# Kernel optimization log

Measured on AMD Instinct MI355X. Metric: run time of the kernel, lower is better.

## Reference

```python
import jax, jax.numpy as jnp
import numpy as np

H = 8        # attention heads
EPS = 1e-5   # LayerNorm eps (torch default)


def _ln(x, g, b):
    m = x.mean(-1, keepdims=True)
    v = ((x - m) ** 2).mean(-1, keepdims=True)
    return (x - m) / jnp.sqrt(v + EPS) * g + b


def _mha(q, k, v):
    # q,k,v: [B, A, S, D] -> attend over S within each (B, A); D = H * dh
    Bq, A, S, Dm = q.shape
    dh = Dm // H
    q = q.reshape(Bq, A, S, H, dh)
    k = k.reshape(Bq, A, S, H, dh)
    v = v.reshape(Bq, A, S, H, dh)
    sc = jnp.einsum('bashe,bathe->bahst', q, k) / jnp.sqrt(jnp.asarray(dh, q.dtype))
    a = jax.nn.softmax(sc, axis=-1)
    o = jnp.einsum('bahst,bathe->bashe', a, v)
    return o.reshape(Bq, A, S, Dm)


def setup_inputs() -> dict:
    Ps, B, C, L, D, DF, PRED = 6, 16, 8, 64, 512, 2048, 96
    key = jax.random.key(0)
    ks = jax.random.split(key, 16)
    g = lambda k, s: jax.random.normal(k, s, jnp.float32) * 0.02
    D2 = (D, D)
    return dict(
        expert_x=jax.random.normal(ks[0], (Ps, B, C, L, D), jnp.float32),
        gates=jax.random.uniform(ks[1], (B, Ps), dtype=jnp.float32),
        cWq=g(ks[2], D2), cbq=jnp.zeros(D), cWk=g(ks[3], D2), cbk=jnp.zeros(D),
        cWv=g(ks[4], D2), cbv=jnp.zeros(D), cWo=g(ks[5], D2), cbo=jnp.zeros(D),
        iWq=g(ks[6], D2), ibq=jnp.zeros(D), iWk=g(ks[7], D2), ibk=jnp.zeros(D),
        iWv=g(ks[8], D2), ibv=jnp.zeros(D), iWo=g(ks[9], D2), ibo=jnp.zeros(D),
        mW1=g(ks[10], (D, DF)), mb1=jnp.zeros(DF),
        mW2=g(ks[11], (DF, D)), mb2=jnp.zeros(D),
        g1=jnp.ones(D), b1=jnp.zeros(D),
        g3=jnp.ones(D), b3=jnp.zeros(D),
        g4=jnp.ones(D), b4=jnp.zeros(D),
        hW=g(ks[12], (D, PRED)), hb=jnp.zeros(PRED),
    )


def reference(expert_x, gates,
              cWq, cbq, cWk, cbk, cWv, cbv, cWo, cbo,
              iWq, ibq, iWk, ibk, iWv, ibv, iWo, ibo,
              mW1, mb1, mW2, mb2,
              g1, b1, g3, b3, g4, b4,
              hW, hb):
    def layer(x):  # x: [B, C, L, D]
        # cross-dimension attention block (attend along L per channel)
        q = x @ cWq + cbq
        k = x @ cWk + cbk
        v = x @ cWv + cbv
        o = _mha(q, k, v) @ cWo + cbo
        x = _ln(x + o, g1, b1)
        # inter-periodicity attention block (rearrange B C L D -> B L C D, attend along C)
        q = (x @ iWq + ibq).swapaxes(1, 2)
        k = (x @ iWk + ibk).swapaxes(1, 2)
        v = (x @ iWv + ibv).swapaxes(1, 2)
        o = _mha(q, k, v).swapaxes(1, 2) @ iWo + ibo
        x = _ln(x + o, g3, b3)
        # inter-periodicity MLP (relu) + residual + norm4
        h = jnp.maximum(x @ mW1 + mb1, 0.0) @ mW2 + mb2
        return _ln(x + h, g4, b4)

    enc = jax.vmap(layer)(expert_x)                      # [Ps, B, C, L, D]
    last = enc[:, :, :, -1, :]                           # [Ps, B, C, D]: xs[i][:, :, -1:, :]
    combined = jnp.einsum('pbcd,bp->bcd', last, gates)   # gated combine over experts
    out = combined @ hW + hb                             # [B, C, pred_len]
    return out.transpose(0, 2, 1)                        # [B, pred_len, C]
```

## Files before the change

kernel.cpp:

```cpp
#include <hip/hip_runtime.h>
#include <hip/hip_bf16.h>

#define NT   49152
#define D_   512
#define DF_  2048
#define PS   6
#define BB   16
#define CC   8
#define LL   64
#define PREDN 96
#define NG   768

typedef unsigned short ushort_t;
using bf16x8 = __attribute__((ext_vector_type(8))) short;
using f32x4  = __attribute__((ext_vector_type(4))) float;

__device__ __forceinline__ float bf2f(unsigned short u) {
  return __uint_as_float((unsigned)u << 16);
}
__device__ __forceinline__ unsigned short f2bf(float f) {
  unsigned u = __float_as_uint(f);
  return (unsigned short)((u + 0x7fffu + ((u >> 16) & 1u)) >> 16);
}
__device__ __forceinline__ void unp2(int x, float& a, float& b) {
  a = __uint_as_float((unsigned)x << 16);
  b = __uint_as_float((unsigned)x & 0xffff0000u);
}
__device__ __forceinline__ void gload16(const void* g, void* l) {
  __builtin_amdgcn_global_load_lds(
      (const __attribute__((address_space(1))) unsigned*)g,
      (__attribute__((address_space(3))) unsigned*)l, 16, 0, 0);
}

template <bool RELU>
__global__ __launch_bounds__(512, 2) void gemm_mfma(
    const ushort_t* __restrict__ A,
    const ushort_t* __restrict__ Bt,
    const float* __restrict__ bias,
    ushort_t* __restrict__ C,
    int M, int N, int K) {
  __shared__ __align__(16) char smem[73728];
  short* lds = (short*)smem;
  const int tid = threadIdx.x;
  const int lane = tid & 63;
  const int w = tid >> 6;
  const int wm = w >> 1;
  const int wn = w & 1;
  const int l15 = lane & 15, l4 = lane >> 4;

  const int nbn = N >> 7;
  const int nwg = gridDim.x;
  const int qq = nwg >> 3, rr = nwg & 7;
  const int xcd = blockIdx.x & 7, within = blockIdx.x >> 3;
  const int wg = (xcd < rr ? xcd * (qq + 1) : rr * (qq + 1) + (xcd - rr) * qq) + within;
  const int bn = (wg % nbn) << 7;
  const int bm = (wg / nbn) << 8;

  const int NKT = K >> 5;

  const int ciA0 = w * 64 + lane;
  const int ciA1 = 512 + w * 64 + lane;
  const int ciB  = w * 64 + lane;
  const int rA0 = ciA0 >> 2, rA1 = ciA1 >> 2, rB = ciB >> 2;
  const int jA0 = (ciA0 & 3) ^ ((rA0 >> 1) & 3);
  const int jA1 = (ciA1 & 3) ^ ((rA1 >> 1) & 3);
  const int jB  = (ciB  & 3) ^ ((rB  >> 1) & 3);
  const ushort_t* gA0 = A + (size_t)(bm + rA0) * K + (jA0 << 3);
  const ushort_t* gA1 = A + (size_t)(bm + rA1) * K + (jA1 << 3);
  const ushort_t* gB  = Bt + (size_t)(bn + rB) * K + (jB << 3);

  auto stage = [&](int st, int sb) {
    const int k0 = st << 5;
    gload16(gA0 + k0, smem + sb * 24576 + w * 1024);
    gload16(gA1 + k0, smem + sb * 24576 + 8192 + w * 1024);
    gload16(gB  + k0, smem + sb * 24576 + 16384 + w * 1024);
  };

  int aconst[4], bconst[4];
#pragma unroll
  for (int m = 0; m < 4; ++m) {
    int row = wm * 64 + m * 16 + l15;
    aconst[m] = row * 32 + ((l4 ^ ((row >> 1) & 3)) << 3);
  }
#pragma unroll
  for (int n = 0; n < 4; ++n) {
    int row = wn * 64 + n * 16 + l15;
    bconst[n] = 8192 + row * 32 + ((l4 ^ ((row >> 1) & 3)) << 3);
  }

  f32x4 acc[4][4] = {};

  stage(0, 0);
  stage(1, 1);

  int rb = 0, sb = 2;
  for (int kt = 0; kt < NKT; ++kt) {
    asm volatile("s_waitcnt vmcnt(3)" ::: "memory");
    __builtin_amdgcn_s_barrier();
    const short* buf = lds + rb * 12288;
    bf16x8 av[4], bv[4];
#pragma unroll
    for (int m = 0; m < 4; ++m) av[m] = *(const bf16x8*)(buf + aconst[m]);
#pragma unroll
    for (int n = 0; n < 4; ++n) bv[n] = *(const bf16x8*)(buf + bconst[n]);
    const int st = (kt + 2 < NKT) ? kt + 2 : NKT - 1;
    stage(st, sb);
    __builtin_amdgcn_s_barrier();
    __builtin_amdgcn_s_setprio(1);
#pragma unroll
    for (int m = 0; m < 4; ++m)
#pragma unroll
      for (int n = 0; n < 4; ++n)
        acc[m][n] = __builtin_amdgcn_mfma_f32_16x16x32_bf16(av[m], bv[n], acc[m][n], 0, 0, 0);
    __builtin_amdgcn_s_setprio(0);
    rb = (rb == 2) ? 0 : rb + 1;
    sb = (sb == 2) ? 0 : sb + 1;
  }

  asm volatile("s_waitcnt vmcnt(0)" ::: "memory");
  __syncthreads();

  float bc[4];
#pragma unroll
  for (int n = 0; n < 4; ++n) bc[n] = bias[bn + wn * 64 + n * 16 + l15];
  short* Cs = lds;
#pragma unroll
  for (int m = 0; m < 4; ++m)
#pragma unroll
    for (int n = 0; n < 4; ++n)
#pragma unroll
      for (int r2 = 0; r2 < 4; ++r2) {
        float v = acc[m][n][r2] + bc[n];
        if (RELU) v = fmaxf(v, 0.f);
        Cs[(wm * 64 + m * 16 + l4 * 4 + r2) * 136 + wn * 64 + n * 16 + l15] =
            (short)f2bf(v);
      }
  __syncthreads();
#pragma unroll
  for (int it = 0; it < 8; ++it) {
    int chunk = it * 512 + tid;
    int r = chunk >> 4;
    int c = (chunk & 15) << 3;
    int4 v = *(const int4*)(Cs + r * 136 + c);
    *(int4*)(C + (size_t)(bm + r) * N + bn + c) = v;
  }
}

__global__ __launch_bounds__(256) void transpose8(
    const float* s0, const float* s1, const float* s2, const float* s3,
    const float* s4, const float* s5, const float* s6, const float* s7,
    ushort_t* d0, ushort_t* d1, ushort_t* d2, ushort_t* d3,
    ushort_t* d4, ushort_t* d5, ushort_t* d6, ushort_t* d7) {
  const float* srcs[8] = {s0, s1, s2, s3, s4, s5, s6, s7};
  ushort_t* dsts[8] = {d0, d1, d2, d3, d4, d5, d6, d7};
  const float* __restrict__ W = srcs[blockIdx.z];
  ushort_t* __restrict__ Wt = dsts[blockIdx.z];
  __shared__ float tile[32][33];
  const int k0 = blockIdx.x * 32, n0 = blockIdx.y * 32;
  const int tx = threadIdx.x & 31, ty = threadIdx.x >> 5;
#pragma unroll
  for (int i = 0; i < 4; ++i)
    tile[ty + i * 8][tx] = W[(size_t)(k0 + ty + i * 8) * 512 + n0 + tx];
  __syncthreads();
#pragma unroll
  for (int i = 0; i < 4; ++i)
    Wt[(size_t)(n0 + ty + i * 8) * 512 + k0 + tx] = f2bf(tile[tx][ty + i * 8]);
}

__global__ __launch_bounds__(256) void transpose_bf16(
    const float* __restrict__ W, ushort_t* __restrict__ Wt, int K, int N) {
  __shared__ float tile[32][33];
  const int k0 = blockIdx.x * 32, n0 = blockIdx.y * 32;
  const int tx = threadIdx.x & 31, ty = threadIdx.x >> 5;
#pragma unroll
  for (int i = 0; i < 4; ++i)
    tile[ty + i * 8][tx] = W[(size_t)(k0 + ty + i * 8) * N + n0 + tx];
  __syncthreads();
#pragma unroll
  for (int i = 0; i < 4; ++i)
    Wt[(size_t)(n0 + ty + i * 8) * K + k0 + tx] = f2bf(tile[tx][ty + i * 8]);
}

__global__ __launch_bounds__(256) void build_wqk(
    const float* __restrict__ cWk, ushort_t* __restrict__ Wqk) {
  int idx = blockIdx.x * 256 + threadIdx.x;
  int n = idx >> 6;
  int c = (idx & 63) * 8;
  int h = n >> 9, k = n & 511;
  union { unsigned short u[8]; int4 v; } pk;
  if ((c >> 6) == h) {
    float4 a = *(const float4*)(cWk + (size_t)k * 512 + c);
    float4 b = *(const float4*)(cWk + (size_t)k * 512 + c + 4);
    pk.u[0] = f2bf(a.x); pk.u[1] = f2bf(a.y); pk.u[2] = f2bf(a.z); pk.u[3] = f2bf(a.w);
    pk.u[4] = f2bf(b.x); pk.u[5] = f2bf(b.y); pk.u[6] = f2bf(b.z); pk.u[7] = f2bf(b.w);
  } else {
    pk.v = make_int4(0, 0, 0, 0);
  }
  *(int4*)(Wqk + (size_t)n * 512 + c) = pk.v;
}

__global__ __launch_bounds__(256) void bias_pack(
    const float* __restrict__ ibq, const float* __restrict__ ibk,
    const float* __restrict__ ibv, float* __restrict__ biqkv,
    float* __restrict__ qz) {
  int i = blockIdx.x * 256 + threadIdx.x;
  if (i < 512) biqkv[i] = ibq[i];
  else if (i < 1024) biqkv[i] = ibk[i - 512];
  else if (i < 1536) biqkv[i] = ibv[i - 1024];
  else if (i < 1536 + 4096) qz[i - 1536] = 0.f;
}

__global__ __launch_bounds__(64) void gather_conv(
    const float* __restrict__ ex, ushort_t* __restrict__ G) {
  const int g = blockIdx.x, lane = threadIdx.x;
  const float* src = ex + ((size_t)g * 64 + 63) * 512 + lane * 8;
  float4 a = *(const float4*)src, b = *(const float4*)(src + 4);
  union { unsigned short u[8]; int4 v; } pk;
  pk.u[0] = f2bf(a.x); pk.u[1] = f2bf(a.y); pk.u[2] = f2bf(a.z); pk.u[3] = f2bf(a.w);
  pk.u[4] = f2bf(b.x); pk.u[5] = f2bf(b.y); pk.u[6] = f2bf(b.z); pk.u[7] = f2bf(b.w);
  *(int4*)(G + (size_t)g * 512 + lane * 8) = pk.v;
}

__global__ __launch_bounds__(256) void attn_fused(
    const float* __restrict__ ex, const ushort_t* __restrict__ QW,
    ushort_t* __restrict__ Y) {
  __shared__ short xs[64][520];
  __shared__ short qws[8][520];
  __shared__ float ss[8][72];
  __shared__ float ps[8][72];
  const int g = blockIdx.x;
  const int tid = threadIdx.x;

  {
    const float* src = ex + (size_t)g * 64 * 512;
#pragma unroll
    for (int it = 0; it < 16; ++it) {
      int i = it * 256 + tid;
      int r = i >> 6, c = (i & 63) * 8;
      float4 a = *(const float4*)(src + r * 512 + c);
      float4 b = *(const float4*)(src + r * 512 + c + 4);
      union { unsigned short u[8]; int4 v; } pk;
      pk.u[0] = f2bf(a.x); pk.u[1] = f2bf(a.y); pk.u[2] = f2bf(a.z); pk.u[3] = f2bf(a.w);
      pk.u[4] = f2bf(b.x); pk.u[5] = f2bf(b.y); pk.u[6] = f2bf(b.z); pk.u[7] = f2bf(b.w);
      *(int4*)(&xs[r][c]) = pk.v;
    }
    const ushort_t* qsrc = QW + (size_t)g * 4096;
#pragma unroll
    for (int it = 0; it < 2; ++it) {
      int i = it * 256 + tid;
      int h = i >> 6, k0 = (i & 63) * 8;
      *(int4*)(&qws[h][k0]) = *(const int4*)(qsrc + i * 8);
    }
  }
  __syncthreads();

#pragma unroll
  for (int ph = 0; ph < 2; ++ph) {
    int h = tid & 7, t = (tid >> 3) + ph * 32;
    float s0 = 0.f, s1 = 0.f, s2 = 0.f, s3 = 0.f;
    float s4 = 0.f, s5 = 0.f, s6 = 0.f, s7 = 0.f;
#pragma unroll
    for (int k8 = 0; k8 < 64; ++k8) {
      bf16x8 xv = *(const bf16x8*)(&xs[t][k8 * 8]);
      bf16x8 qv = *(const bf16x8*)(&qws[h][k8 * 8]);
      s0 += bf2f((unsigned short)xv[0]) * bf2f((unsigned short)qv[0]);
      s1 += bf2f((unsigned short)xv[1]) * bf2f((unsigned short)qv[1]);
      s2 += bf2f((unsigned short)xv[2]) * bf2f((unsigned short)qv[2]);
      s3 += bf2f((unsigned short)xv[3]) * bf2f((unsigned short)qv[3]);
      s4 += bf2f((unsigned short)xv[4]) * bf2f((unsigned short)qv[4]);
      s5 += bf2f((unsigned short)xv[5]) * bf2f((unsigned short)qv[5]);
      s6 += bf2f((unsigned short)xv[6]) * bf2f((unsigned short)qv[6]);
      s7 += bf2f((unsigned short)xv[7]) * bf2f((unsigned short)qv[7]);
    }
    ss[h][t] = (((s0 + s1) + (s2 + s3)) + ((s4 + s5) + (s6 + s7))) * 0.125f;
  }
  __syncthreads();

  {
    int h = tid >> 5, t0 = tid & 31;
    float v0 = ss[h][t0], v1 = ss[h][t0 + 32];
    float mx = fmaxf(v0, v1);
#pragma unroll
    for (int o = 16; o > 0; o >>= 1) mx = fmaxf(mx, __shfl_xor(mx, o));
    float e0 = __expf(v0 - mx), e1 = __expf(v1 - mx);
    float sum = e0 + e1;
#pragma unroll
    for (int o = 16; o > 0; o >>= 1) sum += __shfl_xor(sum, o);
    float inv = 1.f / sum;
    ps[h][t0] = e0 * inv;
    ps[h][t0 + 32] = e1 * inv;
  }
  __syncthreads();

  {
    int h = tid >> 5, k0 = (tid & 31) * 16;
    float acc[16] = {};
#pragma unroll
    for (int t = 0; t < 64; ++t) {
      float p = ps[h][t];
      bf16x8 x0 = *(const bf16x8*)(&xs[t][k0]);
      bf16x8 x1 = *(const bf16x8*)(&xs[t][k0 + 8]);
#pragma unroll
      for (int j = 0; j < 8; ++j) {
        acc[j]     += p * bf2f((unsigned short)x0[j]);
        acc[8 + j] += p * bf2f((unsigned short)x1[j]);
      }
    }
    union { unsigned short u[16]; int4 v[2]; } pk;
#pragma unroll
    for (int j = 0; j < 16; ++j) pk.u[j] = f2bf(acc[j]);
    ushort_t* dst = Y + ((size_t)g * 8 + h) * 512 + k0;
    *(int4*)dst = pk.v[0];
    *(int4*)(dst + 8) = pk.v[1];
  }
}

__global__ __launch_bounds__(64) void gather_diag(
    const ushort_t* __restrict__ T, ushort_t* __restrict__ O) {
  const int g = blockIdx.x;
  const int n0 = threadIdx.x * 8;
  const int h = n0 >> 6;
  *(int4*)(O + (size_t)g * 512 + n0) =
      *(const int4*)(T + ((size_t)g * 8 + h) * 512 + n0);
}

__global__ __launch_bounds__(64) void attn_ctx(
    const ushort_t* __restrict__ QKV, ushort_t* __restrict__ O) {
  __shared__ float qs[8][72], ks[8][72], vsm[8][72], ps2[8][9];
  const int h = blockIdx.x & 7;
  const int pb = blockIdx.x >> 3;
  const int row0 = pb * 8;
  const int tid = threadIdx.x;
  {
    int c = tid >> 3, dc = (tid & 7) * 8;
    size_t r = (size_t)(row0 + c) * 1536 + h * 64 + dc;
    int4 qv = *(const int4*)(QKV + r);
    int4 kv = *(const int4*)(QKV + r + 512);
    int4 vv = *(const int4*)(QKV + r + 1024);
    unp2(qv.x, qs[c][dc + 0], qs[c][dc + 1]); unp2(qv.y, qs[c][dc + 2], qs[c][dc + 3]);
    unp2(qv.z, qs[c][dc + 4], qs[c][dc + 5]); unp2(qv.w, qs[c][dc + 6], qs[c][dc + 7]);
    unp2(kv.x, ks[c][dc + 0], ks[c][dc + 1]); unp2(kv.y, ks[c][dc + 2], ks[c][dc + 3]);
    unp2(kv.z, ks[c][dc + 4], ks[c][dc + 5]); unp2(kv.w, ks[c][dc + 6], ks[c][dc + 7]);
    unp2(vv.x, vsm[c][dc + 0], vsm[c][dc + 1]); unp2(vv.y, vsm[c][dc + 2], vsm[c][dc + 3]);
    unp2(vv.z, vsm[c][dc + 4], vsm[c][dc + 5]); unp2(vv.w, vsm[c][dc + 6], vsm[c][dc + 7]);
  }
  __syncthreads();
  {
    int i = tid >> 3, t = tid & 7;
    float s = 0.f;
#pragma unroll
    for (int d = 0; d < 64; ++d) s += qs[i][d] * ks[t][d];
    ps2[i][t] = s * 0.125f;
  }
  __syncthreads();
  if (tid < 8) {
    float mx = -1e30f;
#pragma unroll
    for (int t = 0; t < 8; ++t) mx = fmaxf(mx, ps2[tid][t]);
    float sum = 0.f;
#pragma unroll
    for (int t = 0; t < 8; ++t) { float e = __expf(ps2[tid][t] - mx); ps2[tid][t] = e; sum += e; }
    float inv = 1.f / sum;
#pragma unroll
    for (int t = 0; t < 8; ++t) ps2[tid][t] *= inv;
  }
  __syncthreads();
#pragma unroll
  for (int c = 0; c < 8; ++c) {
    float s = 0.f;
#pragma unroll
    for (int t = 0; t < 8; ++t) s += ps2[c][t] * vsm[t][tid];
    O[(size_t)(row0 + c) * 512 + h * 64 + tid] = f2bf(s);
  }
}

template <bool INF32>
__global__ __launch_bounds__(256) void add_ln(
    const void* Xin, size_t in_stride, size_t in_base,
    const ushort_t* T, ushort_t* Xout,
    const float* __restrict__ g, const float* __restrict__ b) {
  const size_t off = (size_t)blockIdx.x * D_;
  const size_t ioff = (size_t)blockIdx.x * in_stride + in_base;
  const int tid = threadIdx.x;
  float x0, x1;
  if (INF32) {
    float2 xv = ((const float2*)((const float*)Xin + ioff))[tid];
    x0 = xv.x; x1 = xv.y;
  } else {
    ushort2 xv = ((const ushort2*)((const ushort_t*)Xin + ioff))[tid];
    x0 = bf2f(xv.x); x1 = bf2f(xv.y);
  }
  ushort2 tv = ((const ushort2*)(T + off))[tid];
  x0 += bf2f(tv.x);
  x1 += bf2f(tv.y);
  float s = x0 + x1, q = x0 * x0 + x1 * x1;
#pragma unroll
  for (int o = 32; o > 0; o >>= 1) { s += __shfl_down(s, o); q += __shfl_down(q, o); }
  __shared__ float ssum[4], sqsum[4];
  if ((tid & 63) == 0) { ssum[tid >> 6] = s; sqsum[tid >> 6] = q; }
  __syncthreads();
  float S = ssum[0] + ssum[1] + ssum[2] + ssum[3];
  float Qs = sqsum[0] + sqsum[1] + sqsum[2] + sqsum[3];
  float m = S * (1.f / D_);
  float var = Qs * (1.f / D_) - m * m;
  float inv = rsqrtf(var + 1e-5f);
  float y0 = (x0 - m) * inv * g[tid * 2] + b[tid * 2];
  float y1 = (x1 - m) * inv * g[tid * 2 + 1] + b[tid * 2 + 1];
  ushort2 ov; ov.x = f2bf(y0); ov.y = f2bf(y1);
  ((ushort2*)(Xout + off))[tid] = ov;
}

__global__ __launch_bounds__(256) void final_fuse(
    const ushort_t* __restrict__ X, const ushort_t* __restrict__ P,
    const float* __restrict__ gates,
    const float* __restrict__ g4, const float* __restrict__ b4,
    const float* __restrict__ hW, const float* __restrict__ hb,
    float* __restrict__ out) {
  __shared__ float xr[D_];
  __shared__ float ssum[4], sqsum[4];
  const int bb = blockIdx.x >> 3, cc = blockIdx.x & 7;
  const int tid = threadIdx.x;
  const float gw0 = g4[tid * 2], gw1 = g4[tid * 2 + 1];
  const float bw0 = b4[tid * 2], bw1 = b4[tid * 2 + 1];
  float a0 = 0.f, a1 = 0.f;
#pragma unroll
  for (int p = 0; p < PS; ++p) {
    const size_t row = ((size_t)(p * BB + bb) * CC + cc) * D_;
    ushort2 xv = ((const ushort2*)(X + row))[tid];
    ushort2 tv = ((const ushort2*)(P + row))[tid];
    float x0 = bf2f(xv.x) + bf2f(tv.x);
    float x1 = bf2f(xv.y) + bf2f(tv.y);
    float s = x0 + x1, q = x0 * x0 + x1 * x1;
#pragma unroll
    for (int o = 32; o > 0; o >>= 1) { s += __shfl_down(s, o); q += __shfl_down(q, o); }
    if ((tid & 63) == 0) { ssum[tid >> 6] = s; sqsum[tid >> 6] = q; }
    __syncthreads();
    float S = ssum[0] + ssum[1] + ssum[2] + ssum[3];
    float Qs = sqsum[0] + sqsum[1] + sqsum[2] + sqsum[3];
    float m = S * (1.f / D_);
    float var = Qs * (1.f / D_) - m * m;
    float inv = rsqrtf(var + 1e-5f);
    float gate = gates[bb * PS + p];
    a0 += gate * ((x0 - m) * inv * gw0 + bw0);
    a1 += gate * ((x1 - m) * inv * gw1 + bw1);
    __syncthreads();
  }
  xr[tid * 2] = a0;
  xr[tid * 2 + 1] = a1;
  __syncthreads();
  if (tid < PREDN) {
    float s = hb[tid];
    for (int d = 0; d < D_; ++d) s += xr[d] * hW[d * PREDN + tid];
    out[((size_t)bb * PREDN + tid) * CC + cc] = s;
  }
}

extern "C" void kernel_launch(void* const* d_in, const int* in_sizes, int n_in,
                              void* d_out, int out_size, void* d_ws, size_t ws_size,
                              hipStream_t stream) {
  const float* ex    = (const float*)d_in[0];
  const float* gates = (const float*)d_in[1];
  const float* cWq = (const float*)d_in[2];  const float* cbq = (const float*)d_in[3];
  const float* cWk = (const float*)d_in[4];  const float* cbk = (const float*)d_in[5];
  const float* cWv = (const float*)d_in[6];  const float* cbv = (const float*)d_in[7];
  const float* cWo = (const float*)d_in[8];  const float* cbo = (const float*)d_in[9];
  const float* iWq = (const float*)d_in[10]; const float* ibq = (const float*)d_in[11];
  const float* iWk = (const float*)d_in[12]; const float* ibk = (const float*)d_in[13];
  const float* iWv = (const float*)d_in[14]; const float* ibv = (const float*)d_in[15];
  const float* iWo = (const float*)d_in[16]; const float* ibo = (const float*)d_in[17];
  const float* mW1 = (const float*)d_in[18]; const float* mb1 = (const float*)d_in[19];
  const float* mW2 = (const float*)d_in[20]; const float* mb2 = (const float*)d_in[21];
  const float* g1  = (const float*)d_in[22]; const float* b1  = (const float*)d_in[23];
  const float* g3  = (const float*)d_in[24]; const float* b3  = (const float*)d_in[25];
  const float* g4  = (const float*)d_in[26]; const float* b4  = (const float*)d_in[27];
  const float* hW  = (const float*)d_in[28]; const float* hb  = (const float*)d_in[29];
  float* out = (float*)d_out;

  ushort_t* wq    = (ushort_t*)d_ws;
  ushort_t* wv    = wq + 262144;
  ushort_t* wo    = wv + 262144;
  ushort_t* wiqkv = wo + 262144;
  ushort_t* wio   = wiqkv + 786432;
  ushort_t* w1    = wio + 262144;
  ushort_t* w2    = w1 + 1048576;
  ushort_t* Wqk   = w2 + 1048576;
  float* biqkv = (float*)(Wqk + 2097152);
  float* qz    = biqkv + 1536;
  ushort_t* G768   = (ushort_t*)(qz + 4096);
  ushort_t* Q768   = G768 + (size_t)NG * 512;
  ushort_t* QW     = Q768 + (size_t)NG * 512;
  ushort_t* Yb     = QW + (size_t)NG * 4096;
  ushort_t* Tbuf   = Yb + (size_t)NG * 4096;
  ushort_t* O768   = Tbuf + (size_t)NG * 4096;
  ushort_t* P768   = O768 + (size_t)NG * 512;
  ushort_t* X768   = P768 + (size_t)NG * 512;
  ushort_t* QKV768 = X768 + (size_t)NG * 512;
  ushort_t* H768   = QKV768 + (size_t)NG * 1536;

  transpose8<<<dim3(16, 16, 7), 256, 0, stream>>>(
      cWq, cWv, cWo, iWq, iWk, iWv, iWo, cWq,
      wq, wv, wo, wiqkv, wiqkv + 262144, wiqkv + 524288, wio, wq);
  build_wqk<<<dim3(1024), 256, 0, stream>>>(cWk, Wqk);
  transpose_bf16<<<dim3(16, 64), 256, 0, stream>>>(mW1, w1, 512, 2048);
  transpose_bf16<<<dim3(64, 16), 256, 0, stream>>>(mW2, w2, 2048, 512);
  bias_pack<<<dim3(22), 256, 0, stream>>>(ibq, ibk, ibv, biqkv, qz);

  gather_conv<<<dim3(NG), dim3(64), 0, stream>>>(ex, G768);
  gemm_mfma<false><<<dim3(3 * 4), dim3(512), 0, stream>>>(G768, wq, cbq, Q768, NG, 512, 512);
  gemm_mfma<false><<<dim3(3 * 32), dim3(512), 0, stream>>>(Q768, Wqk, qz, QW, NG, 4096, 512);
  attn_fused<<<dim3(NG), dim3(256), 0, stream>>>(ex, QW, Yb);
  gemm_mfma<false><<<dim3(24 * 4), dim3(512), 0, stream>>>(Yb, wv, cbv, Tbuf, NG * 8, 512, 512);
  gather_diag<<<dim3(NG), dim3(64), 0, stream>>>(Tbuf, O768);
  gemm_mfma<false><<<dim3(3 * 4), dim3(512), 0, stream>>>(O768, wo, cbo, P768, NG, 512, 512);
  add_ln<true><<<dim3(NG), dim3(256), 0, stream>>>(
      ex, (size_t)(LL * D_), (size_t)((LL - 1) * D_), P768, X768, g1, b1);

  gemm_mfma<false><<<dim3(3 * 12), dim3(512), 0, stream>>>(X768, wiqkv, biqkv, QKV768, NG, 1536, 512);
  attn_ctx<<<dim3(96 * 8), dim3(64), 0, stream>>>(QKV768, O768);
  gemm_mfma<false><<<dim3(3 * 4), dim3(512), 0, stream>>>(O768, wio, ibo, P768, NG, 512, 512);
  add_ln<false><<<dim3(NG), dim3(256), 0, stream>>>(
      X768, (size_t)D_, (size_t)0, P768, X768, g3, b3);

  gemm_mfma<true ><<<dim3(3 * 16), dim3(512), 0, stream>>>(X768, w1, mb1, H768, NG, 2048, 512);
  gemm_mfma<false><<<dim3(3 * 4), dim3(512), 0, stream>>>(H768, w2, mb2, P768, NG, 512, 2048);

  final_fuse<<<dim3(BB * CC), dim3(256), 0, stream>>>(
      X768, P768, gates, g4, b4, hW, hb, out);
}
```

Baseline: 212.7 us.

## Use MFMA for attention scores and widen attn_fused to 512 threads

The per-token score dot products (64 tokens x 8 heads x 512) in attn_fused move from scalar FMA loops to bf16 MFMA 16x16x32 instructions on four waves. The 8 heads are padded to 16 rows and the unused half is discarded. The block grows to 512 threads so each wave handles one head in the probability-weighted sum over x, with half the per-thread accumulators. The intent is to cut the VALU-bound score phase and raise parallelism in a kernel that only reads the full 64x512 expert tile, at the cost of wasted MFMA rows and idle waves during the score and softmax phases.

```diff
diff --git a/kernel.cpp b/kernel.cpp
--- a/kernel.cpp
+++ b/kernel.cpp
@@ -221,7 +221,7 @@
   *(int4*)(G + (size_t)g * 512 + lane * 8) = pk.v;
 }
 
-__global__ __launch_bounds__(256) void attn_fused(
+__global__ __launch_bounds__(512, 4) void attn_fused(
     const float* __restrict__ ex, const ushort_t* __restrict__ QW,
     ushort_t* __restrict__ Y) {
   __shared__ short xs[64][520];
@@ -230,12 +230,14 @@
   __shared__ float ps[8][72];
   const int g = blockIdx.x;
   const int tid = threadIdx.x;
+  const int lane = tid & 63;
+  const int w = tid >> 6;
 
   {
     const float* src = ex + (size_t)g * 64 * 512;
 #pragma unroll
-    for (int it = 0; it < 16; ++it) {
-      int i = it * 256 + tid;
+    for (int it = 0; it < 8; ++it) {
+      int i = it * 512 + tid;
       int r = i >> 6, c = (i & 63) * 8;
       float4 a = *(const float4*)(src + r * 512 + c);
       float4 b = *(const float4*)(src + r * 512 + c + 4);
@@ -244,39 +246,33 @@
       pk.u[4] = f2bf(b.x); pk.u[5] = f2bf(b.y); pk.u[6] = f2bf(b.z); pk.u[7] = f2bf(b.w);
       *(int4*)(&xs[r][c]) = pk.v;
     }
-    const ushort_t* qsrc = QW + (size_t)g * 4096;
-#pragma unroll
-    for (int it = 0; it < 2; ++it) {
-      int i = it * 256 + tid;
-      int h = i >> 6, k0 = (i & 63) * 8;
-      *(int4*)(&qws[h][k0]) = *(const int4*)(qsrc + i * 8);
+    int h = tid >> 6, k0 = (tid & 63) * 8;
+    *(int4*)(&qws[h][k0]) = *(const int4*)(QW + (size_t)g * 4096 + tid * 8);
+  }
+  __syncthreads();
+
+  if (w < 4) {
+    f32x4 acc = {0.f, 0.f, 0.f, 0.f};
+    const int arow = lane & 7;
+    const int koff = (lane >> 4) * 8;
+    const short* xrow = &xs[16 * w + (lane & 15)][0];
+#pragma unroll
+    for (int ks = 0; ks < 16; ++ks) {
+      bf16x8 av = *(const bf16x8*)(&qws[arow][ks * 32 + koff]);
+      bf16x8 bv = *(const bf16x8*)(xrow + ks * 32 + koff);
+      acc = __builtin_amdgcn_mfma_f32_16x16x32_bf16(av, bv, acc, 0, 0, 0);
     }
-  }
-  __syncthreads();
-
-#pragma unroll
-  for (int ph = 0; ph < 2; ++ph) {
-    int h = tid & 7, t = (tid >> 3) + ph * 32;
-    float s0 = 0.f, s1 = 0.f, s2 = 0.f, s3 = 0.f;
-    float s4 = 0.f, s5 = 0.f, s6 = 0.f, s7 = 0.f;
-#pragma unroll
-    for (int k8 = 0; k8 < 64; ++k8) {
-      bf16x8 xv = *(const bf16x8*)(&xs[t][k8 * 8]);
-      bf16x8 qv = *(const bf16x8*)(&qws[h][k8 * 8]);
-      s0 += bf2f((unsigned short)xv[0]) * bf2f((unsigned short)qv[0]);
-      s1 += bf2f((unsigned short)xv[1]) * bf2f((unsigned short)qv[1]);
-      s2 += bf2f((unsigned short)xv[2]) * bf2f((unsigned short)qv[2]);
-      s3 += bf2f((unsigned short)xv[3]) * bf2f((unsigned short)qv[3]);
-      s4 += bf2f((unsigned short)xv[4]) * bf2f((unsigned short)qv[4]);
-      s5 += bf2f((unsigned short)xv[5]) * bf2f((unsigned short)qv[5]);
-      s6 += bf2f((unsigned short)xv[6]) * bf2f((unsigned short)qv[6]);
-      s7 += bf2f((unsigned short)xv[7]) * bf2f((unsigned short)qv[7]);
+    int t = 16 * w + (lane & 15);
+    int hbase = (lane >> 4) * 4;
+#pragma unroll
+    for (int r = 0; r < 4; ++r) {
+      int h = hbase + r;
+      if (h < 8) ss[h][t] = acc[r] * 0.125f;
     }
-    ss[h][t] = (((s0 + s1) + (s2 + s3)) + ((s4 + s5) + (s6 + s7))) * 0.125f;
-  }
-  __syncthreads();
-
-  {
+  }
+  __syncthreads();
+
+  if (tid < 256) {
     int h = tid >> 5, t0 = tid & 31;
     float v0 = ss[h][t0], v1 = ss[h][t0 + 32];
     float mx = fmaxf(v0, v1);
@@ -293,25 +289,19 @@
   __syncthreads();
 
   {
-    int h = tid >> 5, k0 = (tid & 31) * 16;
-    float acc[16] = {};
+    const int k0 = lane * 8;
+    float acc[8] = {};
 #pragma unroll
     for (int t = 0; t < 64; ++t) {
-      float p = ps[h][t];
-      bf16x8 x0 = *(const bf16x8*)(&xs[t][k0]);
-      bf16x8 x1 = *(const bf16x8*)(&xs[t][k0 + 8]);
-#pragma unroll
-      for (int j = 0; j < 8; ++j) {
-        acc[j]     += p * bf2f((unsigned short)x0[j]);
-        acc[8 + j] += p * bf2f((unsigned short)x1[j]);
-      }
+      float p = ps[w][t];
+      bf16x8 xv = *(const bf16x8*)(&xs[t][k0]);
+#pragma unroll
+      for (int j = 0; j < 8; ++j) acc[j] += p * bf2f((unsigned short)xv[j]);
     }
-    union { unsigned short u[16]; int4 v[2]; } pk;
-#pragma unroll
-    for (int j = 0; j < 16; ++j) pk.u[j] = f2bf(acc[j]);
-    ushort_t* dst = Y + ((size_t)g * 8 + h) * 512 + k0;
-    *(int4*)dst = pk.v[0];
-    *(int4*)(dst + 8) = pk.v[1];
+    union { unsigned short u[8]; int4 v; } pk;
+#pragma unroll
+    for (int j = 0; j < 8; ++j) pk.u[j] = f2bf(acc[j]);
+    *(int4*)(Y + ((size_t)g * 8 + w) * 512 + k0) = pk.v;
   }
 }
 
@@ -508,7 +498,7 @@
   gather_conv<<<dim3(NG), dim3(64), 0, stream>>>(ex, G768);
   gemm_mfma<false><<<dim3(3 * 4), dim3(512), 0, stream>>>(G768, wq, cbq, Q768, NG, 512, 512);
   gemm_mfma<false><<<dim3(3 * 32), dim3(512), 0, stream>>>(Q768, Wqk, qz, QW, NG, 4096, 512);
-  attn_fused<<<dim3(NG), dim3(256), 0, stream>>>(ex, QW, Yb);
+  attn_fused<<<dim3(NG), dim3(512), 0, stream>>>(ex, QW, Yb);
   gemm_mfma<false><<<dim3(24 * 4), dim3(512), 0, stream>>>(Yb, wv, cbv, Tbuf, NG * 8, 512, 512);
   gather_diag<<<dim3(NG), dim3(64), 0, stream>>>(Tbuf, O768);
   gemm_mfma<false><<<dim3(3 * 4), dim3(512), 0, stream>>>(O768, wo, cbo, P768, NG, 512, 512);
```

New measurement: 194.6 us. 8.5% less time.
